# Optimization experiments

Hardware: AMD Instinct MI355X
Metric: run time of the kernel (lower is better)

The kernel has to match this reference:

```python
import jax, jax.numpy as jnp
import numpy as np

ALPHA = 0.01
EPSB = ALPHA / (1.0 - 2.0 * ALPHA)  # boundary_eps
BIG = 1e9  # stands in for +inf; all real boundary distances are << box diameter


def setup_inputs() -> dict:
    key = jax.random.key(0)
    ks = jax.random.split(key, 8)
    B, D, K = 32768, 16, 1024
    return {
        "x": jax.random.normal(ks[0], (B, D), jnp.float32),
        "logp": jnp.zeros((B, 1), jnp.float32),
        "an1_w": 0.1 * jax.random.normal(ks[1], (D,), jnp.float32),
        "an1_b": 0.1 * jax.random.normal(ks[2], (D,), jnp.float32),
        "an2_w": 0.1 * jax.random.normal(ks[3], (D,), jnp.float32),
        "an2_b": 0.1 * jax.random.normal(ks[4], (D,), jnp.float32),
        "shift_coeff": jax.random.normal(ks[5], (D,), jnp.float32),
        "anchor_raw": jax.random.normal(ks[6], (1, K, D), jnp.float32),  # vorproj._anchor_pts
        "box_min": -4.0 * jnp.ones((D,), jnp.float32),
        "box_max": 4.0 * jnp.ones((D,), jnp.float32),
        "mixture_logits": jnp.zeros((K,), jnp.float32),
    }


def reference(x, logp, an1_w, an1_b, an2_w, an2_b, shift_coeff,
              anchor_raw, box_min, box_max, mixture_logits):
    B, D = x.shape
    # --- actnorm1: y = (x + b) * exp(w); logdet = sum(w) ---
    x = (x + an1_b) * jnp.exp(an1_w)
    logp = logp - jnp.sum(an1_w)
    # --- logit_transform.inverse: y = (sigmoid(x) - alpha) / (1 - 2*alpha) ---
    ld = jnp.sum(jax.nn.log_sigmoid(x) + jax.nn.log_sigmoid(-x), axis=1, keepdims=True) \
         - D * jnp.log(1.0 - 2.0 * ALPHA)
    x = (jax.nn.sigmoid(x) - ALPHA) / (1.0 - 2.0 * ALPHA)
    logp = logp - ld
    # --- (-eps, 1+eps) -> (0, 1) ---
    span = 1.0 + 2.0 * EPSB
    x = (x + EPSB) / span
    logp = logp + D * jnp.log(span)
    # --- scale into box constraints ---
    scale = box_max - box_min  # (D,)
    x = x * scale + box_min
    logp = logp - jnp.sum(jnp.log(scale))
    # --- anchor points: R -> (-1,1) -> (0,1) -> box ---
    a = anchor_raw[0]                       # (K, D)
    a = a / (1.0 + jnp.abs(a))
    a = (a + 1.0) * 0.5 * scale + box_min   # (K, D)
    K = a.shape[0]
    # --- find_nearest: argmin_k ||x - a_k||^2 (drop const ||x||^2) ---
    a_sq = jnp.sum(a * a, axis=1)                    # (K,)
    d2 = a_sq[None, :] - 2.0 * (x @ a.T)             # (B, K)
    k = jnp.argmin(d2, axis=1)                       # (B,)
    mask = jax.nn.one_hot(k, K, dtype=bool).reshape(B, 1, K)
    x_k = a[k]                                       # (B, D) gathered anchor
    # --- shift toward anchor: x + c*(x_k - x); logdet = sum log(1-c) ---
    c = jax.nn.sigmoid(shift_coeff) * 0.98 + 0.01
    x = x + c * (x_k - x)
    logp = logp - jnp.sum(jnp.log1p(-c))
    # --- map_outside_cell: radial map of Voronoi cell (within box) onto R^D ---
    dx = x - x_k
    r = jnp.sqrt(jnp.sum(dx * dx, axis=1))           # (B,)
    u = dx / jnp.maximum(r, 1e-12)[:, None]          # (B, D) unit direction
    # half-plane boundary distance t_j = (||a_j - a_k||^2 / 2) / (u . (a_j - a_k))
    proj = u @ a.T - jnp.sum(u * x_k, axis=1, keepdims=True)              # (B, K)
    halfdist = 0.5 * (a_sq[None, :] + a_sq[k][:, None] - 2.0 * (x_k @ a.T))  # (B, K)
    self_mask = jnp.arange(K)[None, :] == k[:, None]
    valid = jnp.logical_and(jnp.logical_not(self_mask), proj > 1e-12)
    t_half = jnp.where(valid, halfdist / jnp.where(valid, proj, 1.0), BIG)
    # box-face distances along u
    up = u > 1e-12
    un = u < -1e-12
    t_box = jnp.where(up, (box_max[None, :] - x_k) / jnp.where(up, u, 1.0),
            jnp.where(un, (box_min[None, :] - x_k) / jnp.where(un, u, 1.0), BIG))
    t = jnp.minimum(jnp.min(t_half, axis=1), jnp.min(t_box, axis=1))      # (B,)
    ratio = r / t                                     # in [0, 0.99] after shift
    s = 1.0 / (1.0 - ratio)
    x = x_k + dx * s[:, None]
    # logdet = (D+1) * log(t / (t - r)) = -(D+1) * log1p(-ratio)
    logp = logp + (D + 1.0) * jnp.log1p(-ratio)[:, None]
    # --- subtract cell center ---
    x = x - x_k
    # --- actnorm2 ---
    x = (x + an2_b) * jnp.exp(an2_w)
    logp = logp - jnp.sum(an2_w)
    # --- mixture component log-prob ---
    logprobs = jax.nn.log_softmax(mixture_logits)
    logp = logp - logprobs[k][:, None]
    return x, logp, mask
```

## Files before the change

kernel.cpp:

```cpp
#include <hip/hip_runtime.h>
#include <math.h>

#define DD 16
#define KK 1024

typedef float f2 __attribute__((ext_vector_type(2)));

#define WS_A    0
#define WS_ASQ  16384
#define WS_OMC  17408
#define WS_B2   17424
#define WS_E2   17440
#define WS_MN   17456
#define WS_MX   17472
#define WS_SCL  17488
#define WS_DIM  17504
#define WS_E1   17520
#define WS_BASE 17536
#define WS_TOTD 17537
#define WS_NEED_BYTES (WS_TOTD * 8)

__device__ __forceinline__ double xformD(double rv, double mn, double scl) {
  double t = rv / (1.0 + fabs(rv));
  return (t + 1.0) * 0.5 * scl + mn;
}
__device__ __forceinline__ float xformF(float v, float mn, float mx) {
  return (v / (1.f + fabsf(v)) + 1.f) * 0.5f * (mx - mn) + mn;
}

__global__ __launch_bounds__(256) void vor_pre(
    const float* __restrict__ an1_w, const float* __restrict__ an2_w,
    const float* __restrict__ an2_b, const float* __restrict__ shift_c,
    const float* __restrict__ anchor_raw,
    const float* __restrict__ box_min, const float* __restrict__ box_max,
    const float* __restrict__ mlogits, double* __restrict__ ws)
{
  __shared__ double redD[16];
  const int tid = threadIdx.x;
  const int blk = blockIdx.x;

  if (blk == 0 && tid < DD) {
    double w1 = (double)an1_w[tid], w2 = (double)an2_w[tid];
    double sgc = 1.0 / (1.0 + exp(-(double)shift_c[tid]));
    double c = sgc * 0.98 + 0.01;
    double mn = (double)box_min[tid], mx = (double)box_max[tid];
    ws[WS_OMC + tid] = 1.0 - c;
    ws[WS_B2  + tid] = (double)an2_b[tid];
    ws[WS_E2  + tid] = exp(w2);
    ws[WS_MN  + tid] = mn;
    ws[WS_MX  + tid] = mx;
    ws[WS_SCL + tid] = mx - mn;
    ws[WS_E1  + tid] = exp(w1);
    ws[WS_DIM + tid] = -w1 - log(mx - mn) - log1p(-c) - w2;
  }
  const int j0 = blk * 64;
  for (int e = tid; e < 64 * DD; e += 256) {
    int j = j0 + (e >> 4), d = e & 15;
    double mn = (double)box_min[d];
    double scl = (double)box_max[d] - mn;
    ws[WS_A + (size_t)j * DD + d] = xformD((double)anchor_raw[j * DD + d], mn, scl);
  }
  __syncthreads();
  for (int j = j0 + tid; j < j0 + 64; j += 256) {
    double s = 0.0;
    #pragma unroll
    for (int d = 0; d < DD; ++d) { double a = ws[WS_A + (size_t)j * DD + d]; s = fma(a, a, s); }
    ws[WS_ASQ + j] = s;
  }
  if (blk != 0) return;
  float lm = -3.4e38f;
  for (int i = tid; i < KK; i += 256) lm = fmaxf(lm, mlogits[i]);
  #pragma unroll
  for (int o = 32; o > 0; o >>= 1) lm = fmaxf(lm, __shfl_xor(lm, o));
  if ((tid & 63) == 0) redD[tid >> 6] = (double)lm;
  __syncthreads();
  float gmax = (float)fmax(fmax(redD[0], redD[1]), fmax(redD[2], redD[3]));
  double lsum = 0.0;
  for (int i = tid; i < KK; i += 256) lsum += exp((double)mlogits[i] - (double)gmax);
  #pragma unroll
  for (int o = 32; o > 0; o >>= 1) lsum += __shfl_xor(lsum, o);
  if ((tid & 63) == 0) redD[4 + (tid >> 6)] = lsum;
  __syncthreads();
  if (tid == 0) {
    double lse = (double)gmax + log(redD[4] + redD[5] + redD[6] + redD[7]);
    double b = (double)DD * (log(0.98) + log(1.0 + 2.0 * (0.01 / 0.98)));
    #pragma unroll
    for (int d = 0; d < DD; ++d) b += ws[WS_DIM + d];
    ws[WS_BASE] = b + lse;
  }
}

#define NT2 1024
#define RPB2 128
#define NSL 16
#define JSL 64

__global__ __launch_bounds__(NT2, 4) void vor7(
    const float* __restrict__ x_in, const float* __restrict__ logp_in,
    const float* __restrict__ an1_b,
    const float* __restrict__ mlogits, const double* __restrict__ ws,
    float* __restrict__ out, int Brows)
{
  __shared__ __align__(16) float sAp[KK][DD];
  __shared__ float  sAsqH[KK];
  __shared__ double sX4D[DD][RPB2];
  __shared__ float  sLT[DD][RPB2];
  __shared__ double sD2[NSL][RPB2];
  __shared__ int    sJJ[NSL][RPB2];
  __shared__ float  sRat[NSL][RPB2];
  __shared__ float  sOmcF[DD], sB2F[DD], sE2F[DD], sMnF[DD], sMxF[DD];

  const int tid  = threadIdx.x;
  const int w    = tid >> 6;
  const int lane = tid & 63;
  const int r0   = lane, r1 = lane + 64;
  const int row0 = blockIdx.x * RPB2 + r0;
  const int row1 = blockIdx.x * RPB2 + r1;
  const size_t coreEnd = (size_t)Brows * (DD + 1);

  if (tid < DD) {
    sOmcF[tid] = (float)ws[WS_OMC + tid];
    sB2F[tid]  = (float)ws[WS_B2 + tid];
    sE2F[tid]  = (float)ws[WS_E2 + tid];
    sMnF[tid]  = (float)ws[WS_MN + tid];
    sMxF[tid]  = (float)ws[WS_MX + tid];
  }
  for (int e = tid; e < KK * DD; e += NT2) {
    int j = e >> 4, d = e & 15;
    float v = (float)ws[WS_A + (size_t)j * DD + d];
    int pos = (d < 8) ? (2 * d) : (2 * (d - 8) + 1);
    sAp[j][pos] = v;
  }
  {
    const double A = 0.01, EPSB = 0.01 / 0.98;
    const double SPAN = 1.0 + 2.0 * EPSB;
    const float* xb = x_in + (size_t)blockIdx.x * RPB2 * DD;
    for (int e = tid; e < RPB2 * DD; e += NT2) {
      int rr = e >> 4, d = e & 15;
      double y1 = ((double)xb[e] + (double)an1_b[d]) * ws[WS_E1 + d];
      double sg = 1.0 / (1.0 + exp(-y1));
      double x2 = (sg - A) / (1.0 - 2.0 * A);
      double x3 = (x2 + EPSB) / SPAN;
      double x4 = x3 * ws[WS_SCL + d] + ws[WS_MN + d];
      sX4D[d][rr] = x4;
      double ay = fabs(y1);
      sLT[d][rr] = (float)(ay + 2.0 * log1p(exp(-ay)));
    }
  }
  {
    float4* mz = (float4*)(out + coreEnd + (size_t)blockIdx.x * RPB2 * KK);
    #pragma unroll 4
    for (int i = tid; i < RPB2 * KK / 4; i += NT2)
      mz[i] = make_float4(0.f, 0.f, 0.f, 0.f);
  }
  __syncthreads();

  for (int j = tid; j < KK; j += NT2) {
    float a[DD];
    #pragma unroll
    for (int i = 0; i < 8; ++i) { a[i] = sAp[j][2 * i]; a[i + 8] = sAp[j][2 * i + 1]; }
    float acc = 0.f;
    #pragma unroll
    for (int d = 0; d < DD; ++d) acc = fmaf(a[d], a[d], acc);
    sAsqH[j] = 0.5f * acc;
  }

  float x4f0[DD], x4f1[DD];
  #pragma unroll
  for (int d = 0; d < DD; ++d) { x4f0[d] = (float)sX4D[d][r0]; x4f1[d] = (float)sX4D[d][r1]; }
  f2 xp0[8], xp1[8];
  #pragma unroll
  for (int i = 0; i < 8; ++i) {
    xp0[i] = (f2){x4f0[i], x4f0[i + 8]};
    xp1[i] = (f2){x4f1[i], x4f1[i + 8]};
  }
  __syncthreads();

  const int jlo = w * JSL, jhi = jlo + JSL;
  float m1_0 = -3.4e38f, m2_0 = -3.4e38f; int j1_0 = jlo, j2_0 = jlo;
  float m1_1 = -3.4e38f, m2_1 = -3.4e38f; int j1_1 = jlo, j2_1 = jlo;
  #pragma unroll 2
  for (int j = jlo; j < jhi; ++j) {
    const float4* ar = (const float4*)&sAp[j][0];
    float4 A0 = ar[0], A1 = ar[1], A2 = ar[2], A3 = ar[3];
    f2 p0 = (f2){A0.x, A0.y}, p1 = (f2){A0.z, A0.w};
    f2 p2 = (f2){A1.x, A1.y}, p3 = (f2){A1.z, A1.w};
    f2 p4 = (f2){A2.x, A2.y}, p5 = (f2){A2.z, A2.w};
    f2 p6 = (f2){A3.x, A3.y}, p7 = (f2){A3.z, A3.w};
    float nq = -sAsqH[j];
    f2 a0 = (f2){nq, 0.f}, a1 = (f2){nq, 0.f};
    a0 = __builtin_elementwise_fma(xp0[0], p0, a0); a1 = __builtin_elementwise_fma(xp1[0], p0, a1);
    a0 = __builtin_elementwise_fma(xp0[1], p1, a0); a1 = __builtin_elementwise_fma(xp1[1], p1, a1);
    a0 = __builtin_elementwise_fma(xp0[2], p2, a0); a1 = __builtin_elementwise_fma(xp1[2], p2, a1);
    a0 = __builtin_elementwise_fma(xp0[3], p3, a0); a1 = __builtin_elementwise_fma(xp1[3], p3, a1);
    a0 = __builtin_elementwise_fma(xp0[4], p4, a0); a1 = __builtin_elementwise_fma(xp1[4], p4, a1);
    a0 = __builtin_elementwise_fma(xp0[5], p5, a0); a1 = __builtin_elementwise_fma(xp1[5], p5, a1);
    a0 = __builtin_elementwise_fma(xp0[6], p6, a0); a1 = __builtin_elementwise_fma(xp1[6], p6, a1);
    a0 = __builtin_elementwise_fma(xp0[7], p7, a0); a1 = __builtin_elementwise_fma(xp1[7], p7, a1);
    float s0 = a0.x + a0.y, s1 = a1.x + a1.y;
    bool g1 = s0 > m1_0, g2 = s0 > m2_0;
    m2_0 = g1 ? m1_0 : (g2 ? s0 : m2_0);
    j2_0 = g1 ? j1_0 : (g2 ? j : j2_0);
    m1_0 = g1 ? s0 : m1_0;
    j1_0 = g1 ? j : j1_0;
    bool h1b = s1 > m1_1, h2b = s1 > m2_1;
    m2_1 = h1b ? m1_1 : (h2b ? s1 : m2_1);
    j2_1 = h1b ? j1_1 : (h2b ? j : j2_1);
    m1_1 = h1b ? s1 : m1_1;
    j1_1 = h1b ? j : j1_1;
  }

  {
    double bD = 1e300; int bk = 0x7fffffff;
    #pragma unroll
    for (int t = 0; t < 2; ++t) {
      int j = t ? j2_0 : j1_0;
      const double* aj = ws + WS_A + (size_t)j * DD;
      double dot = 0.0;
      #pragma unroll
      for (int d = 0; d < DD; ++d) dot = fma(sX4D[d][r0], aj[d], dot);
      double d2 = ws[WS_ASQ + j] - 2.0 * dot;
      if (d2 < bD || (d2 == bD && j < bk)) { bD = d2; bk = j; }
    }
    sD2[w][r0] = bD; sJJ[w][r0] = bk;
  }
  {
    double bD = 1e300; int bk = 0x7fffffff;
    #pragma unroll
    for (int t = 0; t < 2; ++t) {
      int j = t ? j2_1 : j1_1;
      const double* aj = ws + WS_A + (size_t)j * DD;
      double dot = 0.0;
      #pragma unroll
      for (int d = 0; d < DD; ++d) dot = fma(sX4D[d][r1], aj[d], dot);
      double d2 = ws[WS_ASQ + j] - 2.0 * dot;
      if (d2 < bD || (d2 == bD && j < bk)) { bD = d2; bk = j; }
    }
    sD2[w][r1] = bD; sJJ[w][r1] = bk;
  }
  __syncthreads();

  int k0 = 0x7fffffff, k1 = 0x7fffffff;
  {
    double kb0 = 1e300, kb1 = 1e300;
    #pragma unroll
    for (int ss = 0; ss < NSL; ++ss) {
      double d0 = sD2[ss][r0]; int jj0 = sJJ[ss][r0];
      if (d0 < kb0 || (d0 == kb0 && jj0 < k0)) { kb0 = d0; k0 = jj0; }
      double d1 = sD2[ss][r1]; int jj1 = sJJ[ss][r1];
      if (d1 < kb1 || (d1 == kb1 && jj1 < k1)) { kb1 = d1; k1 = jj1; }
    }
  }

  float akf0[DD], akf1[DD];
  {
    const float4* ap = (const float4*)&sAp[k0][0];
    float4 K0 = ap[0], K1 = ap[1], K2 = ap[2], K3 = ap[3];
    akf0[0]=K0.x; akf0[8]=K0.y; akf0[1]=K0.z; akf0[9]=K0.w;
    akf0[2]=K1.x; akf0[10]=K1.y; akf0[3]=K1.z; akf0[11]=K1.w;
    akf0[4]=K2.x; akf0[12]=K2.y; akf0[5]=K2.z; akf0[13]=K2.w;
    akf0[6]=K3.x; akf0[14]=K3.y; akf0[7]=K3.z; akf0[15]=K3.w;
  }
  {
    const float4* ap = (const float4*)&sAp[k1][0];
    float4 K0 = ap[0], K1 = ap[1], K2 = ap[2], K3 = ap[3];
    akf1[0]=K0.x; akf1[8]=K0.y; akf1[1]=K0.z; akf1[9]=K0.w;
    akf1[2]=K1.x; akf1[10]=K1.y; akf1[3]=K1.z; akf1[11]=K1.w;
    akf1[4]=K2.x; akf1[12]=K2.y; akf1[5]=K2.z; akf1[13]=K2.w;
    akf1[6]=K3.x; akf1[14]=K3.y; akf1[7]=K3.z; akf1[15]=K3.w;
  }
  float dxf0[DD], dxf1[DD];
  float r2_0 = 0.f, dk_0 = 0.f, r2_1 = 0.f, dk_1 = 0.f;
  #pragma unroll
  for (int d = 0; d < DD; ++d) {
    float dx0 = sOmcF[d] * (x4f0[d] - akf0[d]);
    dxf0[d] = dx0;
    r2_0 = fmaf(dx0, dx0, r2_0);
    dk_0 = fmaf(dx0, akf0[d], dk_0);
    float dx1 = sOmcF[d] * (x4f1[d] - akf1[d]);
    dxf1[d] = dx1;
    r2_1 = fmaf(dx1, dx1, r2_1);
    dk_1 = fmaf(dx1, akf1[d], dk_1);
  }
  const float rf0 = sqrtf(r2_0), rr0 = fmaxf(rf0, 1e-12f), sc0 = rf0 / rr0, ep0 = 1e-12f * rf0;
  const float rf1 = sqrtf(r2_1), rr1 = fmaxf(rf1, 1e-12f), sc1 = rf1 / rr1, ep1 = 1e-12f * rf1;
  const float ah0 = sAsqH[k0], ah1 = sAsqH[k1];

  f2 dxp0[8], dxp1[8], nk0[8], nk1[8];
  #pragma unroll
  for (int i = 0; i < 8; ++i) {
    dxp0[i] = (f2){dxf0[i], dxf0[i + 8]};
    dxp1[i] = (f2){dxf1[i], dxf1[i + 8]};
    nk0[i]  = (f2){-akf0[i], -akf0[i + 8]};
    nk1[i]  = (f2){-akf1[i], -akf1[i + 8]};
  }

  float q1_0 = 0.f, h1_0 = 1.f, q1_1 = 0.f, h1_1 = 1.f;
  for (int j = jlo; j < jhi; ++j) {
    const float4* ar = (const float4*)&sAp[j][0];
    float4 A0 = ar[0], A1 = ar[1], A2 = ar[2], A3 = ar[3];
    f2 p0 = (f2){A0.x, A0.y}, p1 = (f2){A0.z, A0.w};
    f2 p2 = (f2){A1.x, A1.y}, p3 = (f2){A1.z, A1.w};
    f2 p4 = (f2){A2.x, A2.y}, p5 = (f2){A2.z, A2.w};
    f2 p6 = (f2){A3.x, A3.y}, p7 = (f2){A3.z, A3.w};
    float aj = sAsqH[j];
    f2 q0 = (f2){-dk_0, 0.f}, h0 = (f2){ah0 + aj, 0.f};
    f2 q1v = (f2){-dk_1, 0.f}, h1v = (f2){ah1 + aj, 0.f};
    q0 = __builtin_elementwise_fma(dxp0[0], p0, q0); h0 = __builtin_elementwise_fma(nk0[0], p0, h0);
    q1v = __builtin_elementwise_fma(dxp1[0], p0, q1v); h1v = __builtin_elementwise_fma(nk1[0], p0, h1v);
    q0 = __builtin_elementwise_fma(dxp0[1], p1, q0); h0 = __builtin_elementwise_fma(nk0[1], p1, h0);
    q1v = __builtin_elementwise_fma(dxp1[1], p1, q1v); h1v = __builtin_elementwise_fma(nk1[1], p1, h1v);
    q0 = __builtin_elementwise_fma(dxp0[2], p2, q0); h0 = __builtin_elementwise_fma(nk0[2], p2, h0);
    q1v = __builtin_elementwise_fma(dxp1[2], p2, q1v); h1v = __builtin_elementwise_fma(nk1[2], p2, h1v);
    q0 = __builtin_elementwise_fma(dxp0[3], p3, q0); h0 = __builtin_elementwise_fma(nk0[3], p3, h0);
    q1v = __builtin_elementwise_fma(dxp1[3], p3, q1v); h1v = __builtin_elementwise_fma(nk1[3], p3, h1v);
    q0 = __builtin_elementwise_fma(dxp0[4], p4, q0); h0 = __builtin_elementwise_fma(nk0[4], p4, h0);
    q1v = __builtin_elementwise_fma(dxp1[4], p4, q1v); h1v = __builtin_elementwise_fma(nk1[4], p4, h1v);
    q0 = __builtin_elementwise_fma(dxp0[5], p5, q0); h0 = __builtin_elementwise_fma(nk0[5], p5, h0);
    q1v = __builtin_elementwise_fma(dxp1[5], p5, q1v); h1v = __builtin_elementwise_fma(nk1[5], p5, h1v);
    q0 = __builtin_elementwise_fma(dxp0[6], p6, q0); h0 = __builtin_elementwise_fma(nk0[6], p6, h0);
    q1v = __builtin_elementwise_fma(dxp1[6], p6, q1v); h1v = __builtin_elementwise_fma(nk1[6], p6, h1v);
    q0 = __builtin_elementwise_fma(dxp0[7], p7, q0); h0 = __builtin_elementwise_fma(nk0[7], p7, h0);
    q1v = __builtin_elementwise_fma(dxp1[7], p7, q1v); h1v = __builtin_elementwise_fma(nk1[7], p7, h1v);
    {
      float q = q0.x + q0.y, h = h0.x + h0.y;
      bool upd = (j != k0) & (q > ep0) & (q * h1_0 > q1_0 * h);
      q1_0 = upd ? q : q1_0;
      h1_0 = upd ? h : h1_0;
    }
    {
      float q = q1v.x + q1v.y, h = h1v.x + h1v.y;
      bool upd = (j != k1) & (q > ep1) & (q * h1_1 > q1_1 * h);
      q1_1 = upd ? q : q1_1;
      h1_1 = upd ? h : h1_1;
    }
  }
  sRat[w][r0] = sc0 * (q1_0 / h1_0);
  sRat[w][r1] = sc1 * (q1_1 / h1_1);
  __syncthreads();

  if (w == 0) {
    {
      float ratio = rf0 * 1e-9f;
      #pragma unroll
      for (int ss = 0; ss < NSL; ++ss) ratio = fmaxf(ratio, sRat[ss][r0]);
      #pragma unroll
      for (int d = 0; d < DD; ++d) {
        float uf = dxf0[d] / rr0;
        if (uf > 1e-12f)        ratio = fmaxf(ratio, rf0 * uf / (sMxF[d] - akf0[d]));
        else if (uf < -1e-12f)  ratio = fmaxf(ratio, rf0 * uf / (sMnF[d] - akf0[d]));
      }
      float sS = 1.0f / (1.0f - ratio);
      float xo[DD];
      float lsig = 0.f;
      #pragma unroll
      for (int d = 0; d < DD; ++d) {
        xo[d] = (dxf0[d] * sS + sB2F[d]) * sE2F[d];
        lsig += sLT[d][r0];
      }
      float4* xp = (float4*)(out + (size_t)row0 * DD);
      xp[0] = make_float4(xo[0], xo[1], xo[2], xo[3]);
      xp[1] = make_float4(xo[4], xo[5], xo[6], xo[7]);
      xp[2] = make_float4(xo[8], xo[9], xo[10], xo[11]);
      xp[3] = make_float4(xo[12], xo[13], xo[14], xo[15]);
      double lp = (double)logp_in[row0] + ws[WS_BASE] + (double)lsig
                + 17.0 * log1p(-(double)ratio)
                - (double)mlogits[k0];
      out[(size_t)Brows * DD + row0] = (float)lp;
      out[coreEnd + (size_t)row0 * KK + k0] = 1.0f;
    }
    {
      float ratio = rf1 * 1e-9f;
      #pragma unroll
      for (int ss = 0; ss < NSL; ++ss) ratio = fmaxf(ratio, sRat[ss][r1]);
      #pragma unroll
      for (int d = 0; d < DD; ++d) {
        float uf = dxf1[d] / rr1;
        if (uf > 1e-12f)        ratio = fmaxf(ratio, rf1 * uf / (sMxF[d] - akf1[d]));
        else if (uf < -1e-12f)  ratio = fmaxf(ratio, rf1 * uf / (sMnF[d] - akf1[d]));
      }
      float sS = 1.0f / (1.0f - ratio);
      float xo[DD];
      float lsig = 0.f;
      #pragma unroll
      for (int d = 0; d < DD; ++d) {
        xo[d] = (dxf1[d] * sS + sB2F[d]) * sE2F[d];
        lsig += sLT[d][r1];
      }
      float4* xp = (float4*)(out + (size_t)row1 * DD);
      xp[0] = make_float4(xo[0], xo[1], xo[2], xo[3]);
      xp[1] = make_float4(xo[4], xo[5], xo[6], xo[7]);
      xp[2] = make_float4(xo[8], xo[9], xo[10], xo[11]);
      xp[3] = make_float4(xo[12], xo[13], xo[14], xo[15]);
      double lp = (double)logp_in[row1] + ws[WS_BASE] + (double)lsig
                + 17.0 * log1p(-(double)ratio)
                - (double)mlogits[k1];
      out[(size_t)Brows * DD + row1] = (float)lp;
      out[coreEnd + (size_t)row1 * KK + k1] = 1.0f;
    }
  }
}

#define NT 256
#define RPB 64
#define SLC4 4
#define JSL4 (KK / SLC4)

__global__ __launch_bounds__(NT, 2) void vor_green(
    const float* __restrict__ x_in, const float* __restrict__ logp_in,
    const float* __restrict__ an1_w, const float* __restrict__ an1_b,
    const float* __restrict__ an2_w, const float* __restrict__ an2_b,
    const float* __restrict__ shift_c, const float* __restrict__ anchor_raw,
    const float* __restrict__ box_min, const float* __restrict__ box_max,
    const float* __restrict__ mlogits,
    float* __restrict__ out, int Brows)
{
  __shared__ __align__(16) float sA[KK][DD];
  __shared__ float  sAsqH[KK];
  __shared__ float  sX4T[DD][RPB];
  __shared__ int    sPj1[SLC4][RPB], sPj2[SLC4][RPB];
  __shared__ int    sRI1[SLC4][RPB], sRI2[SLC4][RPB];
  __shared__ double sPartD[8];
  __shared__ double sE1D[DD], sB1D[DD], sOmcD[DD], sB2D[DD], sE2D[DD];
  __shared__ double sMnD[DD], sMxD[DD], sSclD[DD], sDimD[DD];
  __shared__ double sBaseD;
  __shared__ int    sKidx[RPB];

  const int tid  = threadIdx.x;
  const int sl   = tid >> 6;
  const int lane = tid & 63;
  const int row  = blockIdx.x * RPB + lane;
  const size_t coreEnd = (size_t)Brows * (DD + 1);

  for (int e = tid; e < KK * DD / 4; e += NT) {
    float4 raw = ((const float4*)anchor_raw)[e];
    float4 bmn = ((const float4*)box_min)[e & 3];
    float4 bmx = ((const float4*)box_max)[e & 3];
    float4 o;
    o.x = xformF(raw.x, bmn.x, bmx.x);
    o.y = xformF(raw.y, bmn.y, bmx.y);
    o.z = xformF(raw.z, bmn.z, bmx.z);
    o.w = xformF(raw.w, bmn.w, bmx.w);
    ((float4*)sA)[e] = o;
  }
  if (tid < DD) {
    double w1 = (double)an1_w[tid];
    sE1D[tid] = exp(w1);
    sB1D[tid] = (double)an1_b[tid];
    double sgc = 1.0 / (1.0 + exp(-(double)shift_c[tid]));
    double c = sgc * 0.98 + 0.01;
    sOmcD[tid] = 1.0 - c;
    double mn = (double)box_min[tid], mx = (double)box_max[tid];
    sMnD[tid] = mn; sMxD[tid] = mx; sSclD[tid] = mx - mn;
    double w2 = (double)an2_w[tid];
    sE2D[tid] = exp(w2);
    sB2D[tid] = (double)an2_b[tid];
    sDimD[tid] = -w1 - log(mx - mn) - log1p(-c) - w2;
  }
  __syncthreads();

  for (int j = tid; j < KK; j += NT) {
    float acc = 0.f;
    #pragma unroll
    for (int d = 0; d < DD; ++d) { float a = sA[j][d]; acc = fmaf(a, a, acc); }
    sAsqH[j] = 0.5f * acc;
  }

  float lm = -3.4e38f;
  for (int i = tid; i < KK; i += NT) lm = fmaxf(lm, mlogits[i]);
  #pragma unroll
  for (int o = 32; o > 0; o >>= 1) lm = fmaxf(lm, __shfl_xor(lm, o));
  if (lane == 0) sPartD[sl] = (double)lm;
  __syncthreads();
  float gmax = (float)fmax(fmax(sPartD[0], sPartD[1]), fmax(sPartD[2], sPartD[3]));
  double lsum = 0.0;
  for (int i = tid; i < KK; i += NT) lsum += exp((double)mlogits[i] - (double)gmax);
  #pragma unroll
  for (int o = 32; o > 0; o >>= 1) lsum += __shfl_xor(lsum, o);
  if (lane == 0) sPartD[4 + sl] = lsum;
  __syncthreads();
  if (tid == 0) {
    double lse = (double)gmax + log(sPartD[4] + sPartD[5] + sPartD[6] + sPartD[7]);
    double b = (double)DD * (log(0.98) + log(1.0 + 2.0 * (0.01 / 0.98)));
    #pragma unroll
    for (int d = 0; d < DD; ++d) b += sDimD[d];
    sBaseD = b + lse;
  }

  double x4d[DD];
  double lsigD = 0.0;
  if (sl == 0) {
    const double A = 0.01, EPSB = 0.01 / 0.98;
    const double SPAN = 1.0 + 2.0 * EPSB;
    const float* xr = x_in + (size_t)row * DD;
    #pragma unroll
    for (int d = 0; d < DD; ++d) {
      double y1 = ((double)xr[d] + sB1D[d]) * sE1D[d];
      double sg = 1.0 / (1.0 + exp(-y1));
      double x2 = (sg - A) / (1.0 - 2.0 * A);
      double x3 = (x2 + EPSB) / SPAN;
      double x4 = x3 * sSclD[d] + sMnD[d];
      x4d[d] = x4;
      sX4T[d][lane] = (float)x4;
      double ay = fabs(y1);
      lsigD += ay + 2.0 * log1p(exp(-ay));
    }
  }
  {
    float4* mz = (float4*)(out + coreEnd + (size_t)blockIdx.x * RPB * KK);
    #pragma unroll 4
    for (int i = tid; i < RPB * KK / 4; i += NT)
      mz[i] = make_float4(0.f, 0.f, 0.f, 0.f);
  }
  __syncthreads();

  float x4f[DD];
  #pragma unroll
  for (int d = 0; d < DD; ++d) x4f[d] = sX4T[d][lane];

  float m1 = -3.4e38f, m2v = -3.4e38f;
  int j1 = 0x7fffffff, j2v = 0x7fffffff;
  const int jlo = sl * JSL4, jhi = jlo + JSL4;
  #pragma unroll 2
  for (int j = jlo; j < jhi; ++j) {
    float acc = -sAsqH[j];
    const float4* ar = (const float4*)&sA[j][0];
    #pragma unroll
    for (int dq = 0; dq < 4; ++dq) {
      float4 a4 = ar[dq];
      acc = fmaf(x4f[4 * dq + 0], a4.x, acc);
      acc = fmaf(x4f[4 * dq + 1], a4.y, acc);
      acc = fmaf(x4f[4 * dq + 2], a4.z, acc);
      acc = fmaf(x4f[4 * dq + 3], a4.w, acc);
    }
    bool gt1 = acc > m1;
    bool gt2 = acc > m2v;
    m2v = gt1 ? m1 : (gt2 ? acc : m2v);
    j2v = gt1 ? j1 : (gt2 ? j : j2v);
    m1  = gt1 ? acc : m1;
    j1  = gt1 ? j : j1;
  }
  sPj1[sl][lane] = j1;
  sPj2[sl][lane] = j2v;
  __syncthreads();

  if (sl == 0) {
    double best = 1e300; int bk = 0x7fffffff;
    #pragma unroll
    for (int ss = 0; ss < SLC4; ++ss) {
      #pragma unroll
      for (int t = 0; t < 2; ++t) {
        int j = t ? sPj2[ss][lane] : sPj1[ss][lane];
        double asq = 0.0, dot = 0.0;
        #pragma unroll
        for (int d = 0; d < DD; ++d) {
          double a = xformD((double)anchor_raw[j * DD + d], sMnD[d], sSclD[d]);
          asq = fma(a, a, asq);
          dot = fma(x4d[d], a, dot);
        }
        double d2 = asq - 2.0 * dot;
        if (d2 < best || (d2 == best && j < bk)) { best = d2; bk = j; }
      }
    }
    sKidx[lane] = bk;
  }
  __syncthreads();

  const int k = sKidx[lane];

  float akf[DD], dxf[DD];
  float r2f = 0.f, dxak = 0.f;
  #pragma unroll
  for (int d = 0; d < DD; ++d) {
    float a = sA[k][d];
    akf[d] = a;
    float dx = (float)sOmcD[d] * (x4f[d] - a);
    dxf[d] = dx;
    r2f  = fmaf(dx, dx, r2f);
    dxak = fmaf(dx, a, dxak);
  }
  const float epsr = 1e-12f * sqrtf(r2f);
  const float asqhk = sAsqH[k];

  float q1 = 0.f, h1 = 1.f, q2 = 0.f, h2 = 1.f;
  int i1 = -1, i2 = -1;
  #pragma unroll 2
  for (int j = jlo; j < jhi; ++j) {
    float q = -dxak;
    float h = asqhk + sAsqH[j];
    const float4* ar = (const float4*)&sA[j][0];
    #pragma unroll
    for (int dq = 0; dq < 4; ++dq) {
      float4 a4 = ar[dq];
      q = fmaf(dxf[4 * dq + 0], a4.x, q);
      q = fmaf(dxf[4 * dq + 1], a4.y, q);
      q = fmaf(dxf[4 * dq + 2], a4.z, q);
      q = fmaf(dxf[4 * dq + 3], a4.w, q);
      h = fmaf(-akf[4 * dq + 0], a4.x, h);
      h = fmaf(-akf[4 * dq + 1], a4.y, h);
      h = fmaf(-akf[4 * dq + 2], a4.z, h);
      h = fmaf(-akf[4 * dq + 3], a4.w, h);
    }
    bool valid = (j != k) & (q > epsr);
    bool b1 = valid && (q * h1 > q1 * h);
    bool b2 = valid && (q * h2 > q2 * h);
    float nq2 = b1 ? q1 : (b2 ? q : q2);
    float nh2 = b1 ? h1 : (b2 ? h : h2);
    int   ni2 = b1 ? i1 : (b2 ? j : i2);
    q1 = b1 ? q : q1; h1 = b1 ? h : h1; i1 = b1 ? j : i1;
    q2 = nq2; h2 = nh2; i2 = ni2;
  }
  sRI1[sl][lane] = i1;
  sRI2[sl][lane] = i2;
  __syncthreads();

  if (sl == 0) {
    double akD[DD], dxD[DD];
    double r2 = 0.0;
    #pragma unroll
    for (int d = 0; d < DD; ++d) {
      double a = xformD((double)anchor_raw[k * DD + d], sMnD[d], sSclD[d]);
      akD[d] = a;
      double dx = sOmcD[d] * (x4d[d] - a);
      dxD[d] = dx;
      r2 = fma(dx, dx, r2);
    }
    double rD = sqrt(r2);
    double rr = fmax(rD, 1e-12);
    double ratio = rD / 1e9;

    #pragma unroll
    for (int ss = 0; ss < SLC4; ++ss) {
      #pragma unroll
      for (int t = 0; t < 2; ++t) {
        int j = t ? sRI2[ss][lane] : sRI1[ss][lane];
        if (j < 0 || j == k) continue;
        double q = 0.0, h = 0.0;
        #pragma unroll
        for (int d = 0; d < DD; ++d) {
          double aj = xformD((double)anchor_raw[j * DD + d], sMnD[d], sSclD[d]);
          double g = aj - akD[d];
          q = fma(dxD[d], g, q);
          h = fma(g, g, h);
        }
        double proj = q / rr;
        if (proj > 1e-12) {
          double cand = rD * proj / (0.5 * h);
          ratio = fmax(ratio, cand);
        }
      }
    }
    #pragma unroll
    for (int d = 0; d < DD; ++d) {
      double u = dxD[d] / rr;
      if (u > 1e-12)        ratio = fmax(ratio, rD * u / (sMxD[d] - akD[d]));
      else if (u < -1e-12)  ratio = fmax(ratio, rD * u / (sMnD[d] - akD[d]));
    }

    double sS = 1.0 / (1.0 - ratio);
    float* xo = out + (size_t)row * DD;
    #pragma unroll
    for (int d = 0; d < DD; ++d) {
      double x7 = dxD[d] * sS;
      double x8 = (x7 + sB2D[d]) * sE2D[d];
      xo[d] = (float)x8;
    }
    double lp = (double)logp_in[row] + sBaseD + lsigD
              + 17.0 * log1p(-ratio)
              - (double)mlogits[k];
    out[(size_t)Brows * DD + row] = (float)lp;
    out[coreEnd + (size_t)row * KK + k] = 1.0f;
  }
}

extern "C" void kernel_launch(void* const* d_in, const int* in_sizes, int n_in,
                              void* d_out, int out_size, void* d_ws, size_t ws_size,
                              hipStream_t stream) {
  (void)n_in; (void)out_size;
  const float* x_in   = (const float*)d_in[0];
  const float* logp   = (const float*)d_in[1];
  const float* an1w   = (const float*)d_in[2];
  const float* an1b   = (const float*)d_in[3];
  const float* an2w   = (const float*)d_in[4];
  const float* an2b   = (const float*)d_in[5];
  const float* shiftc = (const float*)d_in[6];
  const float* anchor = (const float*)d_in[7];
  const float* bmin   = (const float*)d_in[8];
  const float* bmax   = (const float*)d_in[9];
  const float* mlog   = (const float*)d_in[10];
  const int B = in_sizes[0] / DD;

  if (ws_size >= (size_t)WS_NEED_BYTES && d_ws != nullptr && (B % RPB2) == 0) {
    double* ws = (double*)d_ws;
    hipLaunchKernelGGL(vor_pre, dim3(16), dim3(256), 0, stream,
                       an1w, an2w, an2b, shiftc, anchor, bmin, bmax, mlog, ws);
    hipLaunchKernelGGL(vor7, dim3(B / RPB2), dim3(NT2), 0, stream,
                       x_in, logp, an1b, mlog,
                       (const double*)ws, (float*)d_out, B);
  } else {
    hipLaunchKernelGGL(vor_green, dim3(B / RPB), dim3(NT), 0, stream,
                       x_in, logp, an1w, an1b, an2w, an2b, shiftc, anchor,
                       bmin, bmax, mlog, (float*)d_out, B);
  }
}
```

Measured before the change: 104.4 us.

## Precompute packed float anchors in prep kernel and distribute box-ratio work across waves

The prep kernel now also writes float anchors in the interleaved shared-memory layout, along with their half squared norms, into the workspace. The main kernel fills shared memory with straight float4 copies and no longer converts from double or recomputes the norms in every block. The per-row box-face ratio and dx computation moves out of the wave-0 epilogue: every wave computes it and folds it into its slice result, so wave 0 only reduces. Unroll factors change and register live ranges are restructured, which may change register pressure and occupancy.

```diff
diff --git a/kernel.cpp b/kernel.cpp
--- a/kernel.cpp
+++ b/kernel.cpp
@@ -17,7 +17,9 @@
 #define WS_DIM  17504
 #define WS_E1   17520
 #define WS_BASE 17536
-#define WS_TOTD 17537
+#define WS_AFP  17538
+#define WS_ASQF 25730
+#define WS_TOTD 26242
 #define WS_NEED_BYTES (WS_TOTD * 8)
 
 __device__ __forceinline__ double xformD(double rv, double mn, double scl) {
@@ -38,6 +40,8 @@
   __shared__ double redD[16];
   const int tid = threadIdx.x;
   const int blk = blockIdx.x;
+  float* aFp   = (float*)(ws + WS_AFP);
+  float* asqHF = (float*)(ws + WS_ASQF);
 
   if (blk == 0 && tid < DD) {
     double w1 = (double)an1_w[tid], w2 = (double)an2_w[tid];
@@ -63,9 +67,22 @@
   __syncthreads();
   for (int j = j0 + tid; j < j0 + 64; j += 256) {
     double s = 0.0;
-    #pragma unroll
-    for (int d = 0; d < DD; ++d) { double a = ws[WS_A + (size_t)j * DD + d]; s = fma(a, a, s); }
+    float af[DD];
+    float accf = 0.f;
+    #pragma unroll
+    for (int d = 0; d < DD; ++d) {
+      double a = ws[WS_A + (size_t)j * DD + d];
+      s = fma(a, a, s);
+      af[d] = (float)a;
+      accf = fmaf(af[d], af[d], accf);
+    }
     ws[WS_ASQ + j] = s;
+    asqHF[j] = 0.5f * accf;
+    #pragma unroll
+    for (int d = 0; d < DD; ++d) {
+      int pos = (d < 8) ? (2 * d) : (2 * (d - 8) + 1);
+      aFp[j * DD + pos] = af[d];
+    }
   }
   if (blk != 0) return;
   float lm = -3.4e38f;
@@ -92,22 +109,23 @@
 
 #define NT2 1024
 #define RPB2 128
-#define NSL 16
-#define JSL 64
-
-__global__ __launch_bounds__(NT2, 4) void vor7(
+#define NS1 16
+#define JS1 (KK / NS1)
+
+__global__ __launch_bounds__(NT2, 4) void vor12(
     const float* __restrict__ x_in, const float* __restrict__ logp_in,
     const float* __restrict__ an1_b,
     const float* __restrict__ mlogits, const double* __restrict__ ws,
+    const float* __restrict__ aFp, const float* __restrict__ asqHF,
     float* __restrict__ out, int Brows)
 {
   __shared__ __align__(16) float sAp[KK][DD];
   __shared__ float  sAsqH[KK];
   __shared__ double sX4D[DD][RPB2];
   __shared__ float  sLT[DD][RPB2];
-  __shared__ double sD2[NSL][RPB2];
-  __shared__ int    sJJ[NSL][RPB2];
-  __shared__ float  sRat[NSL][RPB2];
+  __shared__ double sD2[NS1][RPB2];
+  __shared__ int    sJJ[NS1][RPB2];
+  __shared__ float  sRat[NS1][RPB2];
   __shared__ float  sOmcF[DD], sB2F[DD], sE2F[DD], sMnF[DD], sMxF[DD];
 
   const int tid  = threadIdx.x;
@@ -125,12 +143,10 @@
     sMnF[tid]  = (float)ws[WS_MN + tid];
     sMxF[tid]  = (float)ws[WS_MX + tid];
   }
-  for (int e = tid; e < KK * DD; e += NT2) {
-    int j = e >> 4, d = e & 15;
-    float v = (float)ws[WS_A + (size_t)j * DD + d];
-    int pos = (d < 8) ? (2 * d) : (2 * (d - 8) + 1);
-    sAp[j][pos] = v;
-  }
+  for (int e = tid; e < KK * DD / 4; e += NT2)
+    ((float4*)sAp)[e] = ((const float4*)aFp)[e];
+  for (int j = tid; j < KK; j += NT2)
+    sAsqH[j] = asqHF[j];
   {
     const double A = 0.01, EPSB = 0.01 / 0.98;
     const double SPAN = 1.0 + 2.0 * EPSB;
@@ -147,96 +163,84 @@
       sLT[d][rr] = (float)(ay + 2.0 * log1p(exp(-ay)));
     }
   }
+  __syncthreads();
+
+  f2 xp0[8], xp1[8];
+  #pragma unroll
+  for (int i = 0; i < 8; ++i) {
+    xp0[i] = (f2){(float)sX4D[i][r0], (float)sX4D[i + 8][r0]};
+    xp1[i] = (f2){(float)sX4D[i][r1], (float)sX4D[i + 8][r1]};
+  }
+
   {
     float4* mz = (float4*)(out + coreEnd + (size_t)blockIdx.x * RPB2 * KK);
     #pragma unroll 4
     for (int i = tid; i < RPB2 * KK / 4; i += NT2)
       mz[i] = make_float4(0.f, 0.f, 0.f, 0.f);
   }
-  __syncthreads();
-
-  for (int j = tid; j < KK; j += NT2) {
-    float a[DD];
-    #pragma unroll
-    for (int i = 0; i < 8; ++i) { a[i] = sAp[j][2 * i]; a[i + 8] = sAp[j][2 * i + 1]; }
-    float acc = 0.f;
-    #pragma unroll
-    for (int d = 0; d < DD; ++d) acc = fmaf(a[d], a[d], acc);
-    sAsqH[j] = 0.5f * acc;
-  }
-
-  float x4f0[DD], x4f1[DD];
-  #pragma unroll
-  for (int d = 0; d < DD; ++d) { x4f0[d] = (float)sX4D[d][r0]; x4f1[d] = (float)sX4D[d][r1]; }
-  f2 xp0[8], xp1[8];
-  #pragma unroll
-  for (int i = 0; i < 8; ++i) {
-    xp0[i] = (f2){x4f0[i], x4f0[i + 8]};
-    xp1[i] = (f2){x4f1[i], x4f1[i + 8]};
-  }
-  __syncthreads();
-
-  const int jlo = w * JSL, jhi = jlo + JSL;
-  float m1_0 = -3.4e38f, m2_0 = -3.4e38f; int j1_0 = jlo, j2_0 = jlo;
-  float m1_1 = -3.4e38f, m2_1 = -3.4e38f; int j1_1 = jlo, j2_1 = jlo;
-  #pragma unroll 2
-  for (int j = jlo; j < jhi; ++j) {
-    const float4* ar = (const float4*)&sAp[j][0];
-    float4 A0 = ar[0], A1 = ar[1], A2 = ar[2], A3 = ar[3];
-    f2 p0 = (f2){A0.x, A0.y}, p1 = (f2){A0.z, A0.w};
-    f2 p2 = (f2){A1.x, A1.y}, p3 = (f2){A1.z, A1.w};
-    f2 p4 = (f2){A2.x, A2.y}, p5 = (f2){A2.z, A2.w};
-    f2 p6 = (f2){A3.x, A3.y}, p7 = (f2){A3.z, A3.w};
-    float nq = -sAsqH[j];
-    f2 a0 = (f2){nq, 0.f}, a1 = (f2){nq, 0.f};
-    a0 = __builtin_elementwise_fma(xp0[0], p0, a0); a1 = __builtin_elementwise_fma(xp1[0], p0, a1);
-    a0 = __builtin_elementwise_fma(xp0[1], p1, a0); a1 = __builtin_elementwise_fma(xp1[1], p1, a1);
-    a0 = __builtin_elementwise_fma(xp0[2], p2, a0); a1 = __builtin_elementwise_fma(xp1[2], p2, a1);
-    a0 = __builtin_elementwise_fma(xp0[3], p3, a0); a1 = __builtin_elementwise_fma(xp1[3], p3, a1);
-    a0 = __builtin_elementwise_fma(xp0[4], p4, a0); a1 = __builtin_elementwise_fma(xp1[4], p4, a1);
-    a0 = __builtin_elementwise_fma(xp0[5], p5, a0); a1 = __builtin_elementwise_fma(xp1[5], p5, a1);
-    a0 = __builtin_elementwise_fma(xp0[6], p6, a0); a1 = __builtin_elementwise_fma(xp1[6], p6, a1);
-    a0 = __builtin_elementwise_fma(xp0[7], p7, a0); a1 = __builtin_elementwise_fma(xp1[7], p7, a1);
-    float s0 = a0.x + a0.y, s1 = a1.x + a1.y;
-    bool g1 = s0 > m1_0, g2 = s0 > m2_0;
-    m2_0 = g1 ? m1_0 : (g2 ? s0 : m2_0);
-    j2_0 = g1 ? j1_0 : (g2 ? j : j2_0);
-    m1_0 = g1 ? s0 : m1_0;
-    j1_0 = g1 ? j : j1_0;
-    bool h1b = s1 > m1_1, h2b = s1 > m2_1;
-    m2_1 = h1b ? m1_1 : (h2b ? s1 : m2_1);
-    j2_1 = h1b ? j1_1 : (h2b ? j : j2_1);
-    m1_1 = h1b ? s1 : m1_1;
-    j1_1 = h1b ? j : j1_1;
-  }
-
+
+  const int jlo = w * JS1, jhi = jlo + JS1;
   {
-    double bD = 1e300; int bk = 0x7fffffff;
-    #pragma unroll
-    for (int t = 0; t < 2; ++t) {
-      int j = t ? j2_0 : j1_0;
-      const double* aj = ws + WS_A + (size_t)j * DD;
-      double dot = 0.0;
-      #pragma unroll
-      for (int d = 0; d < DD; ++d) dot = fma(sX4D[d][r0], aj[d], dot);
-      double d2 = ws[WS_ASQ + j] - 2.0 * dot;
-      if (d2 < bD || (d2 == bD && j < bk)) { bD = d2; bk = j; }
-    }
-    sD2[w][r0] = bD; sJJ[w][r0] = bk;
-  }
-  {
-    double bD = 1e300; int bk = 0x7fffffff;
-    #pragma unroll
-    for (int t = 0; t < 2; ++t) {
-      int j = t ? j2_1 : j1_1;
-      const double* aj = ws + WS_A + (size_t)j * DD;
-      double dot = 0.0;
-      #pragma unroll
-      for (int d = 0; d < DD; ++d) dot = fma(sX4D[d][r1], aj[d], dot);
-      double d2 = ws[WS_ASQ + j] - 2.0 * dot;
-      if (d2 < bD || (d2 == bD && j < bk)) { bD = d2; bk = j; }
-    }
-    sD2[w][r1] = bD; sJJ[w][r1] = bk;
+    float m1_0 = -3.4e38f, m2_0 = -3.4e38f; int j1_0 = jlo, j2_0 = jlo;
+    float m1_1 = -3.4e38f, m2_1 = -3.4e38f; int j1_1 = jlo, j2_1 = jlo;
+    #pragma unroll 4
+    for (int j = jlo; j < jhi; ++j) {
+      const float4* ar = (const float4*)&sAp[j][0];
+      float4 A0 = ar[0], A1 = ar[1], A2 = ar[2], A3 = ar[3];
+      f2 p0 = (f2){A0.x, A0.y}, p1 = (f2){A0.z, A0.w};
+      f2 p2 = (f2){A1.x, A1.y}, p3 = (f2){A1.z, A1.w};
+      f2 p4 = (f2){A2.x, A2.y}, p5 = (f2){A2.z, A2.w};
+      f2 p6 = (f2){A3.x, A3.y}, p7 = (f2){A3.z, A3.w};
+      float nq = -sAsqH[j];
+      f2 a0 = (f2){nq, 0.f}, a1 = (f2){nq, 0.f};
+      a0 = __builtin_elementwise_fma(xp0[0], p0, a0); a1 = __builtin_elementwise_fma(xp1[0], p0, a1);
+      a0 = __builtin_elementwise_fma(xp0[1], p1, a0); a1 = __builtin_elementwise_fma(xp1[1], p1, a1);
+      a0 = __builtin_elementwise_fma(xp0[2], p2, a0); a1 = __builtin_elementwise_fma(xp1[2], p2, a1);
+      a0 = __builtin_elementwise_fma(xp0[3], p3, a0); a1 = __builtin_elementwise_fma(xp1[3], p3, a1);
+      a0 = __builtin_elementwise_fma(xp0[4], p4, a0); a1 = __builtin_elementwise_fma(xp1[4], p4, a1);
+      a0 = __builtin_elementwise_fma(xp0[5], p5, a0); a1 = __builtin_elementwise_fma(xp1[5], p5, a1);
+      a0 = __builtin_elementwise_fma(xp0[6], p6, a0); a1 = __builtin_elementwise_fma(xp1[6], p6, a1);
+      a0 = __builtin_elementwise_fma(xp0[7], p7, a0); a1 = __builtin_elementwise_fma(xp1[7], p7, a1);
+      float s0 = a0.x + a0.y, s1 = a1.x + a1.y;
+      bool g1 = s0 > m1_0, g2 = s0 > m2_0;
+      m2_0 = g1 ? m1_0 : (g2 ? s0 : m2_0);
+      j2_0 = g1 ? j1_0 : (g2 ? j : j2_0);
+      m1_0 = g1 ? s0 : m1_0;
+      j1_0 = g1 ? j : j1_0;
+      bool h1b = s1 > m1_1, h2b = s1 > m2_1;
+      m2_1 = h1b ? m1_1 : (h2b ? s1 : m2_1);
+      j2_1 = h1b ? j1_1 : (h2b ? j : j2_1);
+      m1_1 = h1b ? s1 : m1_1;
+      j1_1 = h1b ? j : j1_1;
+    }
+    {
+      double bD = 1e300; int bk = 0x7fffffff;
+      #pragma unroll
+      for (int t = 0; t < 2; ++t) {
+        int j = t ? j2_0 : j1_0;
+        const double* aj = ws + WS_A + (size_t)j * DD;
+        double dot = 0.0;
+        #pragma unroll
+        for (int d = 0; d < DD; ++d) dot = fma(sX4D[d][r0], aj[d], dot);
+        double d2 = ws[WS_ASQ + j] - 2.0 * dot;
+        if (d2 < bD || (d2 == bD && j < bk)) { bD = d2; bk = j; }
+      }
+      sD2[w][r0] = bD; sJJ[w][r0] = bk;
+    }
+    {
+      double bD = 1e300; int bk = 0x7fffffff;
+      #pragma unroll
+      for (int t = 0; t < 2; ++t) {
+        int j = t ? j2_1 : j1_1;
+        const double* aj = ws + WS_A + (size_t)j * DD;
+        double dot = 0.0;
+        #pragma unroll
+        for (int d = 0; d < DD; ++d) dot = fma(sX4D[d][r1], aj[d], dot);
+        double d2 = ws[WS_ASQ + j] - 2.0 * dot;
+        if (d2 < bD || (d2 == bD && j < bk)) { bD = d2; bk = j; }
+      }
+      sD2[w][r1] = bD; sJJ[w][r1] = bk;
+    }
   }
   __syncthreads();
 
@@ -244,7 +248,7 @@
   {
     double kb0 = 1e300, kb1 = 1e300;
     #pragma unroll
-    for (int ss = 0; ss < NSL; ++ss) {
+    for (int ss = 0; ss < NS1; ++ss) {
       double d0 = sD2[ss][r0]; int jj0 = sJJ[ss][r0];
       if (d0 < kb0 || (d0 == kb0 && jj0 < k0)) { kb0 = d0; k0 = jj0; }
       double d1 = sD2[ss][r1]; int jj1 = sJJ[ss][r1];
@@ -252,50 +256,86 @@
     }
   }
 
-  float akf0[DD], akf1[DD];
+  f2 dxp0[8], dxp1[8], nk0[8], nk1[8];
+  float dk_0, dk_1, rf0, rf1, ep0, ep1, sc0, sc1, rinit0, rinit1;
   {
     const float4* ap = (const float4*)&sAp[k0][0];
     float4 K0 = ap[0], K1 = ap[1], K2 = ap[2], K3 = ap[3];
-    akf0[0]=K0.x; akf0[8]=K0.y; akf0[1]=K0.z; akf0[9]=K0.w;
-    akf0[2]=K1.x; akf0[10]=K1.y; akf0[3]=K1.z; akf0[11]=K1.w;
-    akf0[4]=K2.x; akf0[12]=K2.y; akf0[5]=K2.z; akf0[13]=K2.w;
-    akf0[6]=K3.x; akf0[14]=K3.y; akf0[7]=K3.z; akf0[15]=K3.w;
+    float ak[DD];
+    ak[0]=K0.x; ak[8]=K0.y; ak[1]=K0.z; ak[9]=K0.w;
+    ak[2]=K1.x; ak[10]=K1.y; ak[3]=K1.z; ak[11]=K1.w;
+    ak[4]=K2.x; ak[12]=K2.y; ak[5]=K2.z; ak[13]=K2.w;
+    ak[6]=K3.x; ak[14]=K3.y; ak[7]=K3.z; ak[15]=K3.w;
+    float dxf[DD];
+    float r2f = 0.f, dxak = 0.f;
+    #pragma unroll
+    for (int d = 0; d < DD; ++d) {
+      float x4 = (float)sX4D[d][r0];
+      float dx = sOmcF[d] * (x4 - ak[d]);
+      dxf[d] = dx;
+      r2f  = fmaf(dx, dx, r2f);
+      dxak = fmaf(dx, ak[d], dxak);
+    }
+    rf0 = sqrtf(r2f);
+    float rrf = fmaxf(rf0, 1e-12f);
+    sc0 = rf0 / rrf;
+    ep0 = 1e-12f * rf0;
+    dk_0 = dxak;
+    float ratio = rf0 * 1e-9f;
+    #pragma unroll
+    for (int d = 0; d < DD; ++d) {
+      float uf = dxf[d] / rrf;
+      if (uf > 1e-12f)        ratio = fmaxf(ratio, rf0 * uf / (sMxF[d] - ak[d]));
+      else if (uf < -1e-12f)  ratio = fmaxf(ratio, rf0 * uf / (sMnF[d] - ak[d]));
+    }
+    rinit0 = ratio;
+    #pragma unroll
+    for (int i = 0; i < 8; ++i) {
+      dxp0[i] = (f2){dxf[i], dxf[i + 8]};
+      nk0[i]  = (f2){-ak[i], -ak[i + 8]};
+    }
   }
   {
     const float4* ap = (const float4*)&sAp[k1][0];
     float4 K0 = ap[0], K1 = ap[1], K2 = ap[2], K3 = ap[3];
-    akf1[0]=K0.x; akf1[8]=K0.y; akf1[1]=K0.z; akf1[9]=K0.w;
-    akf1[2]=K1.x; akf1[10]=K1.y; akf1[3]=K1.z; akf1[11]=K1.w;
-    akf1[4]=K2.x; akf1[12]=K2.y; akf1[5]=K2.z; akf1[13]=K2.w;
-    akf1[6]=K3.x; akf1[14]=K3.y; akf1[7]=K3.z; akf1[15]=K3.w;
-  }
-  float dxf0[DD], dxf1[DD];
-  float r2_0 = 0.f, dk_0 = 0.f, r2_1 = 0.f, dk_1 = 0.f;
-  #pragma unroll
-  for (int d = 0; d < DD; ++d) {
-    float dx0 = sOmcF[d] * (x4f0[d] - akf0[d]);
-    dxf0[d] = dx0;
-    r2_0 = fmaf(dx0, dx0, r2_0);
-    dk_0 = fmaf(dx0, akf0[d], dk_0);
-    float dx1 = sOmcF[d] * (x4f1[d] - akf1[d]);
-    dxf1[d] = dx1;
-    r2_1 = fmaf(dx1, dx1, r2_1);
-    dk_1 = fmaf(dx1, akf1[d], dk_1);
-  }
-  const float rf0 = sqrtf(r2_0), rr0 = fmaxf(rf0, 1e-12f), sc0 = rf0 / rr0, ep0 = 1e-12f * rf0;
-  const float rf1 = sqrtf(r2_1), rr1 = fmaxf(rf1, 1e-12f), sc1 = rf1 / rr1, ep1 = 1e-12f * rf1;
+    float ak[DD];
+    ak[0]=K0.x; ak[8]=K0.y; ak[1]=K0.z; ak[9]=K0.w;
+    ak[2]=K1.x; ak[10]=K1.y; ak[3]=K1.z; ak[11]=K1.w;
+    ak[4]=K2.x; ak[12]=K2.y; ak[5]=K2.z; ak[13]=K2.w;
+    ak[6]=K3.x; ak[14]=K3.y; ak[7]=K3.z; ak[15]=K3.w;
+    float dxf[DD];
+    float r2f = 0.f, dxak = 0.f;
+    #pragma unroll
+    for (int d = 0; d < DD; ++d) {
+      float x4 = (float)sX4D[d][r1];
+      float dx = sOmcF[d] * (x4 - ak[d]);
+      dxf[d] = dx;
+      r2f  = fmaf(dx, dx, r2f);
+      dxak = fmaf(dx, ak[d], dxak);
+    }
+    rf1 = sqrtf(r2f);
+    float rrf = fmaxf(rf1, 1e-12f);
+    sc1 = rf1 / rrf;
+    ep1 = 1e-12f * rf1;
+    dk_1 = dxak;
+    float ratio = rf1 * 1e-9f;
+    #pragma unroll
+    for (int d = 0; d < DD; ++d) {
+      float uf = dxf[d] / rrf;
+      if (uf > 1e-12f)        ratio = fmaxf(ratio, rf1 * uf / (sMxF[d] - ak[d]));
+      else if (uf < -1e-12f)  ratio = fmaxf(ratio, rf1 * uf / (sMnF[d] - ak[d]));
+    }
+    rinit1 = ratio;
+    #pragma unroll
+    for (int i = 0; i < 8; ++i) {
+      dxp1[i] = (f2){dxf[i], dxf[i + 8]};
+      nk1[i]  = (f2){-ak[i], -ak[i + 8]};
+    }
+  }
   const float ah0 = sAsqH[k0], ah1 = sAsqH[k1];
 
-  f2 dxp0[8], dxp1[8], nk0[8], nk1[8];
-  #pragma unroll
-  for (int i = 0; i < 8; ++i) {
-    dxp0[i] = (f2){dxf0[i], dxf0[i + 8]};
-    dxp1[i] = (f2){dxf1[i], dxf1[i + 8]};
-    nk0[i]  = (f2){-akf0[i], -akf0[i + 8]};
-    nk1[i]  = (f2){-akf1[i], -akf1[i + 8]};
-  }
-
   float q1_0 = 0.f, h1_0 = 1.f, q1_1 = 0.f, h1_1 = 1.f;
+  #pragma unroll 2
   for (int j = jlo; j < jhi; ++j) {
     const float4* ar = (const float4*)&sAp[j][0];
     float4 A0 = ar[0], A1 = ar[1], A2 = ar[2], A3 = ar[3];
@@ -306,21 +346,21 @@
     float aj = sAsqH[j];
     f2 q0 = (f2){-dk_0, 0.f}, h0 = (f2){ah0 + aj, 0.f};
     f2 q1v = (f2){-dk_1, 0.f}, h1v = (f2){ah1 + aj, 0.f};
-    q0 = __builtin_elementwise_fma(dxp0[0], p0, q0); h0 = __builtin_elementwise_fma(nk0[0], p0, h0);
+    q0 = __builtin_elementwise_fma(dxp0[0], p0, q0);  h0 = __builtin_elementwise_fma(nk0[0], p0, h0);
     q1v = __builtin_elementwise_fma(dxp1[0], p0, q1v); h1v = __builtin_elementwise_fma(nk1[0], p0, h1v);
-    q0 = __builtin_elementwise_fma(dxp0[1], p1, q0); h0 = __builtin_elementwise_fma(nk0[1], p1, h0);
+    q0 = __builtin_elementwise_fma(dxp0[1], p1, q0);  h0 = __builtin_elementwise_fma(nk0[1], p1, h0);
     q1v = __builtin_elementwise_fma(dxp1[1], p1, q1v); h1v = __builtin_elementwise_fma(nk1[1], p1, h1v);
-    q0 = __builtin_elementwise_fma(dxp0[2], p2, q0); h0 = __builtin_elementwise_fma(nk0[2], p2, h0);
+    q0 = __builtin_elementwise_fma(dxp0[2], p2, q0);  h0 = __builtin_elementwise_fma(nk0[2], p2, h0);
     q1v = __builtin_elementwise_fma(dxp1[2], p2, q1v); h1v = __builtin_elementwise_fma(nk1[2], p2, h1v);
-    q0 = __builtin_elementwise_fma(dxp0[3], p3, q0); h0 = __builtin_elementwise_fma(nk0[3], p3, h0);
+    q0 = __builtin_elementwise_fma(dxp0[3], p3, q0);  h0 = __builtin_elementwise_fma(nk0[3], p3, h0);
     q1v = __builtin_elementwise_fma(dxp1[3], p3, q1v); h1v = __builtin_elementwise_fma(nk1[3], p3, h1v);
-    q0 = __builtin_elementwise_fma(dxp0[4], p4, q0); h0 = __builtin_elementwise_fma(nk0[4], p4, h0);
+    q0 = __builtin_elementwise_fma(dxp0[4], p4, q0);  h0 = __builtin_elementwise_fma(nk0[4], p4, h0);
     q1v = __builtin_elementwise_fma(dxp1[4], p4, q1v); h1v = __builtin_elementwise_fma(nk1[4], p4, h1v);
-    q0 = __builtin_elementwise_fma(dxp0[5], p5, q0); h0 = __builtin_elementwise_fma(nk0[5], p5, h0);
+    q0 = __builtin_elementwise_fma(dxp0[5], p5, q0);  h0 = __builtin_elementwise_fma(nk0[5], p5, h0);
     q1v = __builtin_elementwise_fma(dxp1[5], p5, q1v); h1v = __builtin_elementwise_fma(nk1[5], p5, h1v);
-    q0 = __builtin_elementwise_fma(dxp0[6], p6, q0); h0 = __builtin_elementwise_fma(nk0[6], p6, h0);
+    q0 = __builtin_elementwise_fma(dxp0[6], p6, q0);  h0 = __builtin_elementwise_fma(nk0[6], p6, h0);
     q1v = __builtin_elementwise_fma(dxp1[6], p6, q1v); h1v = __builtin_elementwise_fma(nk1[6], p6, h1v);
-    q0 = __builtin_elementwise_fma(dxp0[7], p7, q0); h0 = __builtin_elementwise_fma(nk0[7], p7, h0);
+    q0 = __builtin_elementwise_fma(dxp0[7], p7, q0);  h0 = __builtin_elementwise_fma(nk0[7], p7, h0);
     q1v = __builtin_elementwise_fma(dxp1[7], p7, q1v); h1v = __builtin_elementwise_fma(nk1[7], p7, h1v);
     {
       float q = q0.x + q0.y, h = h0.x + h0.y;
@@ -335,29 +375,25 @@
       h1_1 = upd ? h : h1_1;
     }
   }
-  sRat[w][r0] = sc0 * (q1_0 / h1_0);
-  sRat[w][r1] = sc1 * (q1_1 / h1_1);
+  sRat[w][r0] = fmaxf(rinit0, sc0 * (q1_0 / h1_0));
+  sRat[w][r1] = fmaxf(rinit1, sc1 * (q1_1 / h1_1));
   __syncthreads();
 
   if (w == 0) {
     {
-      float ratio = rf0 * 1e-9f;
-      #pragma unroll
-      for (int ss = 0; ss < NSL; ++ss) ratio = fmaxf(ratio, sRat[ss][r0]);
-      #pragma unroll
-      for (int d = 0; d < DD; ++d) {
-        float uf = dxf0[d] / rr0;
-        if (uf > 1e-12f)        ratio = fmaxf(ratio, rf0 * uf / (sMxF[d] - akf0[d]));
-        else if (uf < -1e-12f)  ratio = fmaxf(ratio, rf0 * uf / (sMnF[d] - akf0[d]));
-      }
+      float ratio = sRat[0][r0];
+      #pragma unroll
+      for (int ss = 1; ss < NS1; ++ss) ratio = fmaxf(ratio, sRat[ss][r0]);
       float sS = 1.0f / (1.0f - ratio);
       float xo[DD];
       float lsig = 0.f;
       #pragma unroll
-      for (int d = 0; d < DD; ++d) {
-        xo[d] = (dxf0[d] * sS + sB2F[d]) * sE2F[d];
-        lsig += sLT[d][r0];
+      for (int i = 0; i < 8; ++i) {
+        xo[i]     = (dxp0[i].x * sS + sB2F[i])     * sE2F[i];
+        xo[i + 8] = (dxp0[i].y * sS + sB2F[i + 8]) * sE2F[i + 8];
       }
+      #pragma unroll
+      for (int d = 0; d < DD; ++d) lsig += sLT[d][r0];
       float4* xp = (float4*)(out + (size_t)row0 * DD);
       xp[0] = make_float4(xo[0], xo[1], xo[2], xo[3]);
       xp[1] = make_float4(xo[4], xo[5], xo[6], xo[7]);
@@ -370,23 +406,19 @@
       out[coreEnd + (size_t)row0 * KK + k0] = 1.0f;
     }
     {
-      float ratio = rf1 * 1e-9f;
-      #pragma unroll
-      for (int ss = 0; ss < NSL; ++ss) ratio = fmaxf(ratio, sRat[ss][r1]);
-      #pragma unroll
-      for (int d = 0; d < DD; ++d) {
-        float uf = dxf1[d] / rr1;
-        if (uf > 1e-12f)        ratio = fmaxf(ratio, rf1 * uf / (sMxF[d] - akf1[d]));
-        else if (uf < -1e-12f)  ratio = fmaxf(ratio, rf1 * uf / (sMnF[d] - akf1[d]));
-      }
+      float ratio = sRat[0][r1];
+      #pragma unroll
+      for (int ss = 1; ss < NS1; ++ss) ratio = fmaxf(ratio, sRat[ss][r1]);
       float sS = 1.0f / (1.0f - ratio);
       float xo[DD];
       float lsig = 0.f;
       #pragma unroll
-      for (int d = 0; d < DD; ++d) {
-        xo[d] = (dxf1[d] * sS + sB2F[d]) * sE2F[d];
-        lsig += sLT[d][r1];
+      for (int i = 0; i < 8; ++i) {
+        xo[i]     = (dxp1[i].x * sS + sB2F[i])     * sE2F[i];
+        xo[i + 8] = (dxp1[i].y * sS + sB2F[i + 8]) * sE2F[i + 8];
       }
+      #pragma unroll
+      for (int d = 0; d < DD; ++d) lsig += sLT[d][r1];
       float4* xp = (float4*)(out + (size_t)row1 * DD);
       xp[0] = make_float4(xo[0], xo[1], xo[2], xo[3]);
       xp[1] = make_float4(xo[4], xo[5], xo[6], xo[7]);
@@ -692,11 +724,13 @@
 
   if (ws_size >= (size_t)WS_NEED_BYTES && d_ws != nullptr && (B % RPB2) == 0) {
     double* ws = (double*)d_ws;
+    const float* aFp   = (const float*)(ws + WS_AFP);
+    const float* asqHF = (const float*)(ws + WS_ASQF);
     hipLaunchKernelGGL(vor_pre, dim3(16), dim3(256), 0, stream,
                        an1w, an2w, an2b, shiftc, anchor, bmin, bmax, mlog, ws);
-    hipLaunchKernelGGL(vor7, dim3(B / RPB2), dim3(NT2), 0, stream,
-                       x_in, logp, an1b, mlog,
-                       (const double*)ws, (float*)d_out, B);
+    hipLaunchKernelGGL(vor12, dim3(B / RPB2), dim3(NT2), 0, stream,
+                       x_in, logp, an1b, mlog, (const double*)ws,
+                       aFp, asqHF, (float*)d_out, B);
   } else {
     hipLaunchKernelGGL(vor_green, dim3(B / RPB), dim3(NT), 0, stream,
                        x_in, logp, an1w, an1b, an2w, an2b, shiftc, anchor,
```

Result: no change. 104.8 us (+0.4%).
